# Optimization experiments

Measured on AMD Instinct MI355X. Metric: run time of the kernel, lower is better.

The kernel has to match this reference:

```python
import jax, jax.numpy as jnp
import numpy as np

S, B, T, D, TS, V = 256, 8, 1024, 512, 512, 32000
LN_EPS = 1e-5


def setup_inputs() -> dict:
    key = jax.random.key(0)
    ks = jax.random.split(key, 16)
    std = 0.02
    inp = {
        "outs": jax.random.normal(ks[0], (S, B, D), jnp.float32),
        "graph_state": jax.random.normal(ks[1], (T, B, D), jnp.float32),
        "graph_padding_mask": jnp.zeros((B, T), bool),
        "copy_seq": jax.random.randint(ks[2], (T, B), 0, V),
        # single-head attention projections
        "Wq": std * jax.random.normal(ks[3], (D, D), jnp.float32),
        "bq": jnp.zeros((D,), jnp.float32),
        "Wk": std * jax.random.normal(ks[4], (D, D), jnp.float32),
        "bk": jnp.zeros((D,), jnp.float32),
        "Wv": std * jax.random.normal(ks[5], (D, D), jnp.float32),
        "bv": jnp.zeros((D,), jnp.float32),
        "Wo": std * jax.random.normal(ks[6], (D, D), jnp.float32),
        "bo": jnp.zeros((D,), jnp.float32),
        # layer norm
        "ln_g": jnp.ones((D,), jnp.float32),
        "ln_b": jnp.zeros((D,), jnp.float32),
        # transfer / generator / diverter linears
        "Wt": std * jax.random.normal(ks[7], (TS, D), jnp.float32),
        "bt": jnp.zeros((TS,), jnp.float32),
        "Wgen": std * jax.random.normal(ks[8], (V, TS), jnp.float32),
        "bgen": jnp.zeros((V,), jnp.float32),
        "Wdiv": std * jax.random.normal(ks[9], (2, TS), jnp.float32),
        "bdiv": jnp.zeros((2,), jnp.float32),
    }
    return inp


def _layer_norm(x, g, b):
    mu = jnp.mean(x, -1, keepdims=True)
    var = jnp.mean(jnp.square(x - mu), -1, keepdims=True)
    return (x - mu) * jax.lax.rsqrt(var + LN_EPS) * g + b


def reference(outs, graph_state, graph_padding_mask, copy_seq,
              Wq, bq, Wk, bk, Wv, bv, Wo, bo, ln_g, ln_b,
              Wt, bt, Wgen, bgen, Wdiv, bdiv):
    scale = 1.0 / jnp.sqrt(jnp.asarray(D, outs.dtype))
    q = (outs @ Wq.T + bq) * scale              # [S,B,D]
    k = graph_state @ Wk.T + bk                 # [T,B,D]
    v = graph_state @ Wv.T + bv                 # [T,B,D]
    scores = jnp.einsum("sbd,tbd->sbt", q, k)   # [S,B,T]
    scores = jnp.where(graph_padding_mask[None, :, :], -1e9, scores)
    attn = jax.nn.softmax(scores, axis=-1)      # alignment_weight [S,B,T]
    ctx = jnp.einsum("sbt,tbd->sbd", attn, v)
    x = ctx @ Wo.T + bo
    outs = _layer_norm(outs + x, ln_g, ln_b)
    outs_token = jnp.tanh(outs @ Wt.T + bt)     # [S,B,TS]
    gates = jax.nn.softmax(outs_token @ Wdiv.T + bdiv, axis=-1)
    gen_gate, copy_gate = gates[..., 0:1], gates[..., 1:2]
    probs = gen_gate * jax.nn.softmax(outs_token @ Wgen.T + bgen, axis=-1)  # [S,B,V]
    # copy indices: [T,B] -> [S,B,T] broadcast (indices < V, so no vocab extension)
    index = jnp.broadcast_to(copy_seq.T[None, :, :], (S, B, T))
    copy_probs = copy_gate * attn               # [S,B,T]
    s_idx = jnp.arange(S)[:, None, None]
    b_idx = jnp.arange(B)[None, :, None]
    probs = probs.at[s_idx, b_idx, index].add(copy_probs)
    ll = jnp.log(probs + 1e-12)
    return ll
```

## Files before the change

### kernel.cpp

```cpp
#include <hip/hip_runtime.h>
#include <hip/hip_bf16.h>
#include <math.h>

#define SS 256
#define BB 8
#define TT 1024
#define DD 512
#define TSD 512
#define VV 32000
#define LN_EPS_F 1e-5f
#define VHALF 16000

typedef __attribute__((ext_vector_type(8))) short bf16x8;
typedef __attribute__((ext_vector_type(4))) float f32x4;

__device__ __forceinline__ unsigned short f2bf(float f) {
    union { float f; unsigned int u; } c; c.f = f;
    unsigned int u = c.u;
    return (unsigned short)((u + 0x7fffu + ((u >> 16) & 1u)) >> 16);
}
__device__ __forceinline__ float bf2f(unsigned short s) {
    union { unsigned int u; float f; } c; c.u = ((unsigned int)s) << 16;
    return c.f;
}

__device__ __forceinline__ void glls16(const void* g, void* l) {
    __builtin_amdgcn_global_load_lds(
        (const __attribute__((address_space(1))) unsigned int*)g,
        (__attribute__((address_space(3))) unsigned int*)l,
        16, 0, 0);
}

__device__ __forceinline__ float warp_red_sum(float v) {
    for (int o = 32; o > 0; o >>= 1) v += __shfl_down(v, o, 64);
    return v;
}
__device__ __forceinline__ float warp_red_max(float v) {
    for (int o = 32; o > 0; o >>= 1) v = fmaxf(v, __shfl_down(v, o, 64));
    return v;
}
__device__ __forceinline__ float block_red_sum(float v, float* s) {
    int lane = threadIdx.x & 63, wid = threadIdx.x >> 6;
    v = warp_red_sum(v);
    __syncthreads();
    if (lane == 0) s[wid] = v;
    __syncthreads();
    float r = 0.f;
    int nw = blockDim.x >> 6;
    for (int i = 0; i < nw; i++) r += s[i];
    return r;
}
__device__ __forceinline__ float block_red_max(float v, float* s) {
    int lane = threadIdx.x & 63, wid = threadIdx.x >> 6;
    v = warp_red_max(v);
    __syncthreads();
    if (lane == 0) s[wid] = v;
    __syncthreads();
    float r = s[0];
    int nw = blockDim.x >> 6;
    for (int i = 1; i < nw; i++) r = fmaxf(r, s[i]);
    return r;
}

template<int IN_BF16, int OUT_MODE, int ACT>
__device__ __forceinline__ void gemm_body(
    unsigned short* smem, int bx, int by, int z,
    const void* __restrict__ Ap, long long lda, long long aoff,
    const void* __restrict__ Bp, long long ldb, long long boff,
    const float* __restrict__ bias,
    void* __restrict__ Cp, long long ldc, long long coff,
    int K, float scale, float* __restrict__ rsum)
{
    unsigned short* As = smem;
    unsigned short* Bs = smem + 128 * 64;
    const int tid = threadIdx.x;
    const int lane = tid & 63;
    const int wave = tid >> 6;
    const int wm = (wave >> 1) << 6;
    const int wn = (wave & 1) << 6;
    const int lane15 = lane & 15;
    const int quad = lane >> 4;
    const long long m0 = (long long)bx * 128;
    const long long n0 = (long long)by * 128;

    f32x4 acc[4][4];
#pragma unroll
    for (int i = 0; i < 4; i++)
#pragma unroll
        for (int j = 0; j < 4; j++) acc[i][j] = (f32x4){0.f, 0.f, 0.f, 0.f};

    for (int k0 = 0; k0 < K; k0 += 64) {
        if (IN_BF16) {
            const unsigned short* A = (const unsigned short*)Ap + z * aoff;
            const unsigned short* B = (const unsigned short*)Bp + z * boff;
#pragma unroll
            for (int r = 0; r < 4; r++) {
                int c = r * 256 + tid;
                int row = c >> 3;
                int kc = (c & 7) ^ (row & 7);
                glls16(A + (m0 + row) * lda + k0 + kc * 8, &As[c * 8]);
                glls16(B + (n0 + row) * ldb + k0 + kc * 8, &Bs[c * 8]);
            }
        } else {
            const float* A = (const float*)Ap + z * aoff;
            const float* B = (const float*)Bp + z * boff;
#pragma unroll
            for (int r = 0; r < 4; r++) {
                int c = r * 256 + tid;
                int row = c >> 3;
                int kc = (c & 7) ^ (row & 7);
                const float* ga = A + (m0 + row) * lda + k0 + kc * 8;
                const float* gb = B + (n0 + row) * ldb + k0 + kc * 8;
                float4 a0 = *(const float4*)ga, a1 = *(const float4*)(ga + 4);
                float4 b0 = *(const float4*)gb, b1 = *(const float4*)(gb + 4);
                union { unsigned short us[8]; int4 v; } pa, pb;
                pa.us[0] = f2bf(a0.x); pa.us[1] = f2bf(a0.y); pa.us[2] = f2bf(a0.z); pa.us[3] = f2bf(a0.w);
                pa.us[4] = f2bf(a1.x); pa.us[5] = f2bf(a1.y); pa.us[6] = f2bf(a1.z); pa.us[7] = f2bf(a1.w);
                pb.us[0] = f2bf(b0.x); pb.us[1] = f2bf(b0.y); pb.us[2] = f2bf(b0.z); pb.us[3] = f2bf(b0.w);
                pb.us[4] = f2bf(b1.x); pb.us[5] = f2bf(b1.y); pb.us[6] = f2bf(b1.z); pb.us[7] = f2bf(b1.w);
                *(int4*)&As[c * 8] = pa.v;
                *(int4*)&Bs[c * 8] = pb.v;
            }
        }
        __syncthreads();
#pragma unroll
        for (int s = 0; s < 2; s++) {
            bf16x8 af[4], bfr[4];
#pragma unroll
            for (int i = 0; i < 4; i++) {
                int arow = wm + i * 16 + lane15;
                int kc = (s * 4 + quad) ^ (lane15 & 7);
                af[i] = *(const bf16x8*)&As[(arow * 8 + kc) * 8];
                int brow = wn + i * 16 + lane15;
                bfr[i] = *(const bf16x8*)&Bs[(brow * 8 + kc) * 8];
            }
#pragma unroll
            for (int i = 0; i < 4; i++)
#pragma unroll
                for (int j = 0; j < 4; j++)
                    acc[i][j] = __builtin_amdgcn_mfma_f32_16x16x32_bf16(af[i], bfr[j], acc[i][j], 0, 0, 0);
        }
        __syncthreads();
    }
    const long long zc = z * coff;
    float* sRowF = (float*)&smem[0];
    if (ACT == 2) {
        if (tid < 128) sRowF[tid] = 0.f;
        __syncthreads();
    }
#pragma unroll
    for (int i = 0; i < 4; i++) {
        float rs[4] = {0.f, 0.f, 0.f, 0.f};
#pragma unroll
        for (int j = 0; j < 4; j++) {
            float bv = bias ? bias[n0 + wn + j * 16 + lane15] : 0.f;
#pragma unroll
            for (int r2 = 0; r2 < 4; r2++) {
                float v = (acc[i][j][r2] + bv) * scale;
                if (ACT == 1) v = tanhf(v);
                if (ACT == 2) { v = __expf(v); rs[r2] += v; }
                acc[i][j][r2] = v;
            }
        }
        if (ACT == 2) {
#pragma unroll
            for (int r2 = 0; r2 < 4; r2++) {
                float s = rs[r2];
                s += __shfl_xor(s, 1, 64);
                s += __shfl_xor(s, 2, 64);
                s += __shfl_xor(s, 4, 64);
                s += __shfl_xor(s, 8, 64);
                if (lane15 == 0) atomicAdd(&sRowF[wm + i * 16 + quad * 4 + r2], s);
            }
        }
    }
    if (ACT == 2) {
        __syncthreads();
        if (tid < 128) atomicAdd(rsum + m0 + tid, sRowF[tid]);
        __syncthreads();
    }
    if (OUT_MODE >= 1) {
#pragma unroll
        for (int i = 0; i < 4; i++) {
#pragma unroll
            for (int r2 = 0; r2 < 4; r2++) {
                int lr = wm + i * 16 + quad * 4 + r2;
                int sw = (lr & 7) << 4;
#pragma unroll
                for (int j = 0; j < 4; j++) {
                    int lc = wn + j * 16 + lane15;
                    smem[lr * 128 + (lc ^ sw)] = f2bf(acc[i][j][r2]);
                }
            }
        }
        __syncthreads();
        if (OUT_MODE == 1) {
            unsigned short* Co = (unsigned short*)Cp + zc;
#pragma unroll
            for (int u = 0; u < 8; u++) {
                int e = tid + u * 256;
                int lr = e >> 4, lc8 = e & 15;
                int lcs = (lc8 * 8) ^ ((lr & 7) << 4);
                int4 vv4 = *(const int4*)&smem[lr * 128 + lcs];
                *(int4*)(Co + (m0 + lr) * ldc + n0 + lc8 * 8) = vv4;
            }
        } else {
            unsigned short* vT = (unsigned short*)Cp;
            const int t0g = (int)(m0 >> 3);
#pragma unroll
            for (int u = 0; u < 4; u++) {
                int e = tid + u * 256;
                int b = e >> 7, dl = e & 127;
                int sw = (b & 7) << 4;
                union { unsigned short us[16]; int4 v[2]; } pk;
#pragma unroll
                for (int tl = 0; tl < 16; tl++)
                    pk.us[tl] = smem[(tl * 8 + b) * 128 + (dl ^ sw)];
                unsigned short* dst = vT + (long long)b * (DD * TT) + (long long)(n0 + dl) * TT + t0g;
                *(int4*)dst = pk.v[0];
                *(int4*)(dst + 8) = pk.v[1];
            }
        }
        __syncthreads();
    } else {
#pragma unroll
        for (int i = 0; i < 4; i++) {
            long long rbase = m0 + wm + i * 16 + quad * 4;
#pragma unroll
            for (int j = 0; j < 4; j++) {
                long long col = n0 + wn + j * 16 + lane15;
#pragma unroll
                for (int r2 = 0; r2 < 4; r2++)
                    ((float*)Cp)[zc + (rbase + r2) * ldc + col] = acc[i][j][r2];
            }
        }
    }
}

template<int IN_BF16, int OUT_MODE, int ACT, int SWZ>
__global__ __launch_bounds__(256) void mfma_gemm(
    const void* __restrict__ Ap, long long lda, long long aoff,
    const void* __restrict__ Bp, long long ldb, long long boff,
    const float* __restrict__ bias,
    void* __restrict__ Cp, long long ldc, long long coff,
    int K, float scale, float* __restrict__ rsum)
{
    __shared__ __align__(16) unsigned short smem[2 * 128 * 64];
    int bx = blockIdx.x, by = blockIdx.y;
    if (SWZ) {
        unsigned int nx = gridDim.x;
        unsigned int nwg = nx * gridDim.y;
        unsigned int lin = blockIdx.y * nx + blockIdx.x;
        unsigned int q = nwg >> 3, r = nwg & 7u;
        unsigned int xcd = lin & 7u, loc = lin >> 3;
        unsigned int wg = (xcd < r ? xcd * (q + 1u) : r * (q + 1u) + (xcd - r) * q) + loc;
        bx = (int)(wg % nx);
        by = (int)(wg / nx);
    }
    gemm_body<IN_BF16, OUT_MODE, ACT>(smem, bx, by, blockIdx.z,
        Ap, lda, aoff, Bp, ldb, boff, bias, Cp, ldc, coff, K, scale, rsum);
}

__global__ __launch_bounds__(256) void front_fused(
    const float* __restrict__ outs, const float* __restrict__ Wq, const float* __restrict__ bq,
    const float* __restrict__ gstate, const float* __restrict__ Wk, const float* __restrict__ bk,
    const float* __restrict__ Wv, const float* __restrict__ bv,
    unsigned short* __restrict__ qb, unsigned short* __restrict__ kb,
    unsigned short* __restrict__ vTb,
    const float* __restrict__ Wgen, unsigned short* __restrict__ wgenb,
    float* __restrict__ gs, float qscale)
{
    extern __shared__ __align__(16) unsigned short dsm[];
    const int bid = blockIdx.x;
    if (bid < 64) {
        gemm_body<0, 1, 0>(dsm, bid & 15, bid >> 4, 0,
            outs, 512, 0, Wq, 512, 0, bq, qb, 512, 0, 512, qscale, nullptr);
    } else if (bid < 320) {
        int lb = bid - 64;
        gemm_body<0, 1, 0>(dsm, lb & 63, lb >> 6, 0,
            gstate, 512, 0, Wk, 512, 0, bk, kb, 512, 0, 512, 1.f, nullptr);
    } else if (bid < 576) {
        int lb = bid - 320;
        gemm_body<0, 2, 0>(dsm, lb & 63, lb >> 6, 0,
            gstate, 512, 0, Wv, 512, 0, bv, vTb, 0, 0, 512, 1.f, nullptr);
    } else {
        int lb = bid - 576;
        if (lb < 8) gs[lb * 256 + threadIdx.x] = 0.f;
        long long i = (long long)lb * 256 + threadIdx.x;
        const float4* p = (const float4*)Wgen + i * 2;
        float4 a = p[0], b = p[1];
        union { unsigned short us[8]; int4 v; } pk;
        pk.us[0] = f2bf(a.x); pk.us[1] = f2bf(a.y); pk.us[2] = f2bf(a.z); pk.us[3] = f2bf(a.w);
        pk.us[4] = f2bf(b.x); pk.us[5] = f2bf(b.y); pk.us[6] = f2bf(b.z); pk.us[7] = f2bf(b.w);
        ((int4*)wgenb)[i] = pk.v;
    }
}

__global__ __launch_bounds__(256) void attn_softmax(
    float* __restrict__ scores, unsigned short* __restrict__ scores_bf,
    const unsigned char* __restrict__ mask)
{
    __shared__ float red[4];
    int row = blockIdx.x;
    int b = row & (BB - 1);
    float* p = scores + (long long)row * TT;
    unsigned short* pb = scores_bf + (long long)row * TT;
    const unsigned char* mr = mask + (long long)b * TT;
    float vals[TT / 256];
    float lmax = -3.0e38f;
#pragma unroll
    for (int i = 0; i < TT / 256; i++) {
        int t = threadIdx.x + i * 256;
        float s = p[t];
        if (mr[t]) s = -1.0e9f;
        vals[i] = s;
        lmax = fmaxf(lmax, s);
    }
    float gmax = block_red_max(lmax, red);
    float lsum = 0.f;
#pragma unroll
    for (int i = 0; i < TT / 256; i++) {
        vals[i] = __expf(vals[i] - gmax);
        lsum += vals[i];
    }
    float gsum = block_red_sum(lsum, red);
    float inv = 1.f / gsum;
#pragma unroll
    for (int i = 0; i < TT / 256; i++) {
        float v = vals[i] * inv;
        int t = threadIdx.x + i * 256;
        p[t] = v;
        pb[t] = f2bf(v);
    }
}

__global__ __launch_bounds__(256) void add_ln(
    const float* __restrict__ outs, const float* __restrict__ xo,
    const float* __restrict__ g, const float* __restrict__ bln,
    float* __restrict__ y)
{
    __shared__ float red[4];
    int row = blockIdx.x;
    const float* o = outs + (long long)row * DD;
    const float* xp = xo + (long long)row * DD;
    float x[DD / 256];
    float s = 0.f;
#pragma unroll
    for (int i = 0; i < DD / 256; i++) {
        int d = threadIdx.x + i * 256;
        x[i] = o[d] + xp[d];
        s += x[i];
    }
    float mu = block_red_sum(s, red) * (1.f / DD);
    float s2 = 0.f;
#pragma unroll
    for (int i = 0; i < DD / 256; i++) {
        float dv = x[i] - mu;
        s2 += dv * dv;
    }
    float var = block_red_sum(s2, red) * (1.f / DD);
    float rinv = rsqrtf(var + LN_EPS_F);
#pragma unroll
    for (int i = 0; i < DD / 256; i++) {
        int d = threadIdx.x + i * 256;
        y[(long long)row * DD + d] = (x[i] - mu) * rinv * g[d] + bln[d];
    }
}

__global__ __launch_bounds__(512) void copy_log_final(
    const unsigned short* __restrict__ eb, const float* __restrict__ attn,
    const unsigned short* __restrict__ tok, const float* __restrict__ Wdiv,
    const float* __restrict__ bdiv, const float* __restrict__ gs,
    const int* __restrict__ seq, float* __restrict__ out)
{
    __shared__ __align__(16) float pc[VHALF];
    __shared__ float red[8];
    const int tid = threadIdx.x;
    const int row = blockIdx.x;
    const int half = blockIdx.y;
    const int base = half * VHALF;
    const int b = row & (BB - 1);

    for (int i = tid; i < VHALF; i += 512) pc[i] = 0.f;

    float tv = bf2f(tok[(long long)row * TSD + tid]);
    float a0 = tv * Wdiv[tid];
    float a1 = tv * Wdiv[TSD + tid];
    a0 = block_red_sum(a0, red);
    a1 = block_red_sum(a1, red);
    a0 += bdiv[0];
    a1 += bdiv[1];
    float mx = fmaxf(a0, a1);
    float e0 = __expf(a0 - mx), e1 = __expf(a1 - mx);
    float inv2 = 1.f / (e0 + e1);
    const float cv = e1 * inv2;
    const float ginv = (e0 * inv2) / gs[row];
    __syncthreads();

    const float* arow = attn + (long long)row * TT;
#pragma unroll
    for (int it = 0; it < 2; it++) {
        int t = tid + it * 512;
        int idx = seq[t * BB + b];
        int loc = idx - base;
        if (loc >= 0 && loc < VHALF)
            atomicAdd(&pc[loc], cv * arow[t]);
    }
    __syncthreads();

    const unsigned short* erow = eb + (long long)row * VV + base;
    float* orow = out + (long long)row * VV + base;
    const float4* pc4 = (const float4*)pc;
    for (int c = tid; c < VHALF / 8; c += 512) {
        bf16x8 ev = *(const bf16x8*)(erow + c * 8);
        float4 p0 = pc4[c * 2], p1 = pc4[c * 2 + 1];
        float4 o0, o1;
        o0.x = __logf(fmaf(bf2f((unsigned short)ev[0]), ginv, p0.x) + 1e-12f);
        o0.y = __logf(fmaf(bf2f((unsigned short)ev[1]), ginv, p0.y) + 1e-12f);
        o0.z = __logf(fmaf(bf2f((unsigned short)ev[2]), ginv, p0.z) + 1e-12f);
        o0.w = __logf(fmaf(bf2f((unsigned short)ev[3]), ginv, p0.w) + 1e-12f);
        o1.x = __logf(fmaf(bf2f((unsigned short)ev[4]), ginv, p1.x) + 1e-12f);
        o1.y = __logf(fmaf(bf2f((unsigned short)ev[5]), ginv, p1.y) + 1e-12f);
        o1.z = __logf(fmaf(bf2f((unsigned short)ev[6]), ginv, p1.z) + 1e-12f);
        o1.w = __logf(fmaf(bf2f((unsigned short)ev[7]), ginv, p1.w) + 1e-12f);
        ((float4*)orow)[c * 2] = o0;
        ((float4*)orow)[c * 2 + 1] = o1;
    }
}

extern "C" void kernel_launch(void* const* d_in, const int* in_sizes, int n_in,
                              void* d_out, int out_size, void* d_ws, size_t ws_size,
                              hipStream_t stream)
{
    const float* outs = (const float*)d_in[0];
    const float* gstate = (const float*)d_in[1];
    const unsigned char* mask = (const unsigned char*)d_in[2];
    const int* seq = (const int*)d_in[3];
    const float* Wq = (const float*)d_in[4];  const float* bq = (const float*)d_in[5];
    const float* Wk = (const float*)d_in[6];  const float* bk = (const float*)d_in[7];
    const float* Wv = (const float*)d_in[8];  const float* bv = (const float*)d_in[9];
    const float* Wo = (const float*)d_in[10]; const float* bo = (const float*)d_in[11];
    const float* lng = (const float*)d_in[12]; const float* lnb = (const float*)d_in[13];
    const float* Wt = (const float*)d_in[14]; const float* bt = (const float*)d_in[15];
    const float* Wgen = (const float*)d_in[16]; const float* bgen = (const float*)d_in[17];
    const float* Wdiv = (const float*)d_in[18]; const float* bdiv = (const float*)d_in[19];
    float* out = (float*)d_out;

    char* w = (char*)d_ws;
    unsigned short* qb    = (unsigned short*)w; w += 2048LL * 512 * 2;
    unsigned short* kb    = (unsigned short*)w; w += 8192LL * 512 * 2;
    unsigned short* tokb  = (unsigned short*)w; w += 2048LL * 512 * 2;
    unsigned short* wgenb = (unsigned short*)w; w += 32000LL * 512 * 2;
    unsigned short* vTb   = (unsigned short*)w; w += 8LL * 512 * 1024 * 2;
    unsigned short* attnb = (unsigned short*)w; w += 2048LL * 1024 * 2;
    unsigned short* eb    = (unsigned short*)w; w += 2048LL * 32000 * 2;
    float* attn = (float*)w; w += 2048LL * 1024 * 4;
    float* ctx  = (float*)w; w += 2048LL * 512 * 4;
    float* xo   = (float*)w; w += 2048LL * 512 * 4;
    float* y    = (float*)w; w += 2048LL * 512 * 4;
    float* gs   = (float*)w; w += 2048 * 4;

    float qscale = 1.0f / sqrtf((float)DD);
    dim3 blk(256);

    front_fused<<<8576, blk, 32768, stream>>>(outs, Wq, bq, gstate, Wk, bk, Wv, bv,
                                              qb, kb, vTb, Wgen, wgenb, gs, qscale);
    mfma_gemm<1, 0, 0, 0><<<dim3(2, 8, 8), blk, 0, stream>>>(qb, 4096, 512, kb, 4096, 512, nullptr, attn, 8192, 1024, 512, 1.f, nullptr);
    attn_softmax<<<2048, blk, 0, stream>>>(attn, attnb, mask);
    mfma_gemm<1, 0, 0, 0><<<dim3(2, 4, 8), blk, 0, stream>>>(attnb, 8192, 1024, vTb, 1024, 524288, nullptr, ctx, 4096, 512, 1024, 1.f, nullptr);
    mfma_gemm<0, 0, 0, 0><<<dim3(16, 4, 1), blk, 0, stream>>>(ctx, 512, 0, Wo, 512, 0, bo, xo, 512, 0, 512, 1.f, nullptr);
    add_ln<<<2048, blk, 0, stream>>>(outs, xo, lng, lnb, y);
    mfma_gemm<0, 1, 1, 0><<<dim3(16, 4, 1), blk, 0, stream>>>(y, 512, 0, Wt, 512, 0, bt, tokb, 512, 0, 512, 1.f, nullptr);
    mfma_gemm<1, 1, 2, 1><<<dim3(16, 250, 1), blk, 0, stream>>>(tokb, 512, 0, wgenb, 512, 0, bgen, eb, 32000, 0, 512, 1.f, gs);
    copy_log_final<<<dim3(2048, 2), dim3(512), 0, stream>>>(eb, attn, tokb, Wdiv, bdiv, gs, seq, out);
}
```

Before: 702.3 us.

## Split-K the attention GEMMs and fuse residual-add LayerNorm into neighbouring GEMMs

The QK^T and attn·V batched GEMMs now use split-K over two halves, writing two partial fp32 buffers to double the block count on small grids. The partials are summed in the softmax load and in the A-load of the Wo GEMM. The Wo GEMM epilogue adds the residual, writes the sum, and atomically accumulates per-row sum and sum-of-squares. The next GEMM then applies LayerNorm on its A tile during load, which removes the separate add_ln kernel. The fp32 attention writeback is dropped and the copy scatter reads bf16 attention, saving traffic at the cost of single-pass variance precision and bf16 copy probabilities.

```diff
diff --git a/kernel.cpp b/kernel.cpp
--- a/kernel.cpp
+++ b/kernel.cpp
@@ -62,14 +62,18 @@
     return r;
 }
 
-template<int IN_BF16, int OUT_MODE, int ACT>
+template<int IN_BF16, int OUT_MODE, int ACT, int LN_A, int DUALA>
 __device__ __forceinline__ void gemm_body(
     unsigned short* smem, int bx, int by, int z,
-    const void* __restrict__ Ap, long long lda, long long aoff,
+    const void* __restrict__ Ap, const void* __restrict__ Ap2,
+    long long lda, long long aoff,
     const void* __restrict__ Bp, long long ldb, long long boff,
     const float* __restrict__ bias,
     void* __restrict__ Cp, long long ldc, long long coff,
-    int K, float scale, float* __restrict__ rsum)
+    int K, float scale, float* __restrict__ rsum, float* __restrict__ rsum2,
+    const float* __restrict__ outsP,
+    const float* __restrict__ lnrs, const float* __restrict__ lnrss,
+    const float* __restrict__ lng, const float* __restrict__ lnbp)
 {
     unsigned short* As = smem;
     unsigned short* Bs = smem + 128 * 64;
@@ -113,6 +117,30 @@
                 const float* gb = B + (n0 + row) * ldb + k0 + kc * 8;
                 float4 a0 = *(const float4*)ga, a1 = *(const float4*)(ga + 4);
                 float4 b0 = *(const float4*)gb, b1 = *(const float4*)(gb + 4);
+                if (DUALA) {
+                    const float* ga2 = (const float*)Ap2 + z * aoff + (m0 + row) * lda + k0 + kc * 8;
+                    float4 c0 = *(const float4*)ga2, c1 = *(const float4*)(ga2 + 4);
+                    a0.x += c0.x; a0.y += c0.y; a0.z += c0.z; a0.w += c0.w;
+                    a1.x += c1.x; a1.y += c1.y; a1.z += c1.z; a1.w += c1.w;
+                }
+                if (LN_A) {
+                    long long grow = m0 + row;
+                    float mu = lnrs[grow] * (1.f / DD);
+                    float var = lnrss[grow] * (1.f / DD) - mu * mu;
+                    float rinv = rsqrtf(var + LN_EPS_F);
+                    const float* gp = lng + k0 + kc * 8;
+                    const float* bp = lnbp + k0 + kc * 8;
+                    float4 g0 = *(const float4*)gp, g1 = *(const float4*)(gp + 4);
+                    float4 e0 = *(const float4*)bp, e1 = *(const float4*)(bp + 4);
+                    a0.x = (a0.x - mu) * rinv * g0.x + e0.x;
+                    a0.y = (a0.y - mu) * rinv * g0.y + e0.y;
+                    a0.z = (a0.z - mu) * rinv * g0.z + e0.z;
+                    a0.w = (a0.w - mu) * rinv * g0.w + e0.w;
+                    a1.x = (a1.x - mu) * rinv * g1.x + e1.x;
+                    a1.y = (a1.y - mu) * rinv * g1.y + e1.y;
+                    a1.z = (a1.z - mu) * rinv * g1.z + e1.z;
+                    a1.w = (a1.w - mu) * rinv * g1.w + e1.w;
+                }
                 union { unsigned short us[8]; int4 v; } pa, pb;
                 pa.us[0] = f2bf(a0.x); pa.us[1] = f2bf(a0.y); pa.us[2] = f2bf(a0.z); pa.us[3] = f2bf(a0.w);
                 pa.us[4] = f2bf(a1.x); pa.us[5] = f2bf(a1.y); pa.us[6] = f2bf(a1.z); pa.us[7] = f2bf(a1.w);
@@ -148,29 +176,51 @@
         if (tid < 128) sRowF[tid] = 0.f;
         __syncthreads();
     }
+    if (ACT == 3) {
+        if (tid < 256) sRowF[tid] = 0.f;
+        __syncthreads();
+    }
 #pragma unroll
     for (int i = 0; i < 4; i++) {
-        float rs[4] = {0.f, 0.f, 0.f, 0.f};
+        const long long rbase = m0 + wm + i * 16 + quad * 4;
+        float rs_[4] = {0.f, 0.f, 0.f, 0.f};
+        float rq_[4] = {0.f, 0.f, 0.f, 0.f};
 #pragma unroll
         for (int j = 0; j < 4; j++) {
-            float bv = bias ? bias[n0 + wn + j * 16 + lane15] : 0.f;
+            long long col = n0 + wn + j * 16 + lane15;
+            float bv = bias ? bias[col] : 0.f;
 #pragma unroll
             for (int r2 = 0; r2 < 4; r2++) {
                 float v = (acc[i][j][r2] + bv) * scale;
                 if (ACT == 1) v = tanhf(v);
-                if (ACT == 2) { v = __expf(v); rs[r2] += v; }
+                if (ACT == 2) { v = __expf(v); rs_[r2] += v; }
+                if (ACT == 3) {
+                    long long idx = zc + (rbase + r2) * ldc + col;
+                    v += outsP[idx];
+                    ((float*)Cp)[idx] = v;
+                    rs_[r2] += v;
+                    rq_[r2] += v * v;
+                }
                 acc[i][j][r2] = v;
             }
         }
-        if (ACT == 2) {
+        if (ACT == 2 || ACT == 3) {
 #pragma unroll
             for (int r2 = 0; r2 < 4; r2++) {
-                float s = rs[r2];
+                float s = rs_[r2];
                 s += __shfl_xor(s, 1, 64);
                 s += __shfl_xor(s, 2, 64);
                 s += __shfl_xor(s, 4, 64);
                 s += __shfl_xor(s, 8, 64);
                 if (lane15 == 0) atomicAdd(&sRowF[wm + i * 16 + quad * 4 + r2], s);
+                if (ACT == 3) {
+                    float q = rq_[r2];
+                    q += __shfl_xor(q, 1, 64);
+                    q += __shfl_xor(q, 2, 64);
+                    q += __shfl_xor(q, 4, 64);
+                    q += __shfl_xor(q, 8, 64);
+                    if (lane15 == 0) atomicAdd(&sRowF[128 + wm + i * 16 + quad * 4 + r2], q);
+                }
             }
         }
     }
@@ -178,6 +228,14 @@
         __syncthreads();
         if (tid < 128) atomicAdd(rsum + m0 + tid, sRowF[tid]);
         __syncthreads();
+    }
+    if (ACT == 3) {
+        __syncthreads();
+        if (tid < 128) {
+            atomicAdd(rsum + m0 + tid, sRowF[tid]);
+            atomicAdd(rsum2 + m0 + tid, sRowF[128 + tid]);
+        }
+        return;
     }
     if (OUT_MODE >= 1) {
 #pragma unroll
@@ -237,13 +295,17 @@
     }
 }
 
-template<int IN_BF16, int OUT_MODE, int ACT, int SWZ>
+template<int IN_BF16, int OUT_MODE, int ACT, int LN_A, int DUALA, int SWZ>
 __global__ __launch_bounds__(256) void mfma_gemm(
-    const void* __restrict__ Ap, long long lda, long long aoff,
+    const void* __restrict__ Ap, const void* __restrict__ Ap2,
+    long long lda, long long aoff,
     const void* __restrict__ Bp, long long ldb, long long boff,
     const float* __restrict__ bias,
     void* __restrict__ Cp, long long ldc, long long coff,
-    int K, float scale, float* __restrict__ rsum)
+    int K, float scale, float* __restrict__ rsum, float* __restrict__ rsum2,
+    const float* __restrict__ outsP,
+    const float* __restrict__ lnrs, const float* __restrict__ lnrss,
+    const float* __restrict__ lng, const float* __restrict__ lnbp)
 {
     __shared__ __align__(16) unsigned short smem[2 * 128 * 64];
     int bx = blockIdx.x, by = blockIdx.y;
@@ -257,8 +319,25 @@
         bx = (int)(wg % nx);
         by = (int)(wg / nx);
     }
-    gemm_body<IN_BF16, OUT_MODE, ACT>(smem, bx, by, blockIdx.z,
-        Ap, lda, aoff, Bp, ldb, boff, bias, Cp, ldc, coff, K, scale, rsum);
+    gemm_body<IN_BF16, OUT_MODE, ACT, LN_A, DUALA>(smem, bx, by, blockIdx.z,
+        Ap, Ap2, lda, aoff, Bp, ldb, boff, bias, Cp, ldc, coff, K, scale,
+        rsum, rsum2, outsP, lnrs, lnrss, lng, lnbp);
+}
+
+__global__ __launch_bounds__(256) void mfma_gemm_splitk(
+    const unsigned short* __restrict__ Ap, long long lda, long long aoff,
+    const unsigned short* __restrict__ Bp, long long ldb, long long boff,
+    float* __restrict__ C0, float* __restrict__ C1,
+    long long ldc, long long coff, int Khalf)
+{
+    __shared__ __align__(16) unsigned short smem[2 * 128 * 64];
+    int b = blockIdx.z & 7, kz = blockIdx.z >> 3;
+    const unsigned short* A = Ap + (long long)kz * Khalf;
+    const unsigned short* B = Bp + (long long)kz * Khalf;
+    float* C = kz ? C1 : C0;
+    gemm_body<1, 0, 0, 0, 0>(smem, blockIdx.x, blockIdx.y, b,
+        A, nullptr, lda, aoff, B, ldb, boff, nullptr, C, ldc, coff, Khalf, 1.f,
+        nullptr, nullptr, nullptr, nullptr, nullptr, nullptr, nullptr);
 }
 
 __global__ __launch_bounds__(256) void front_fused(
@@ -268,24 +347,31 @@
     unsigned short* __restrict__ qb, unsigned short* __restrict__ kb,
     unsigned short* __restrict__ vTb,
     const float* __restrict__ Wgen, unsigned short* __restrict__ wgenb,
-    float* __restrict__ gs, float qscale)
+    float* __restrict__ gs, float* __restrict__ rs, float* __restrict__ rss,
+    float qscale)
 {
     extern __shared__ __align__(16) unsigned short dsm[];
     const int bid = blockIdx.x;
     if (bid < 64) {
-        gemm_body<0, 1, 0>(dsm, bid & 15, bid >> 4, 0,
-            outs, 512, 0, Wq, 512, 0, bq, qb, 512, 0, 512, qscale, nullptr);
+        gemm_body<0, 1, 0, 0, 0>(dsm, bid & 15, bid >> 4, 0,
+            outs, nullptr, 512, 0, Wq, 512, 0, bq, qb, 512, 0, 512, qscale,
+            nullptr, nullptr, nullptr, nullptr, nullptr, nullptr, nullptr);
     } else if (bid < 320) {
         int lb = bid - 64;
-        gemm_body<0, 1, 0>(dsm, lb & 63, lb >> 6, 0,
-            gstate, 512, 0, Wk, 512, 0, bk, kb, 512, 0, 512, 1.f, nullptr);
+        gemm_body<0, 1, 0, 0, 0>(dsm, lb & 63, lb >> 6, 0,
+            gstate, nullptr, 512, 0, Wk, 512, 0, bk, kb, 512, 0, 512, 1.f,
+            nullptr, nullptr, nullptr, nullptr, nullptr, nullptr, nullptr);
     } else if (bid < 576) {
         int lb = bid - 320;
-        gemm_body<0, 2, 0>(dsm, lb & 63, lb >> 6, 0,
-            gstate, 512, 0, Wv, 512, 0, bv, vTb, 0, 0, 512, 1.f, nullptr);
+        gemm_body<0, 2, 0, 0, 0>(dsm, lb & 63, lb >> 6, 0,
+            gstate, nullptr, 512, 0, Wv, 512, 0, bv, vTb, 0, 0, 512, 1.f,
+            nullptr, nullptr, nullptr, nullptr, nullptr, nullptr, nullptr);
     } else {
         int lb = bid - 576;
-        if (lb < 8) gs[lb * 256 + threadIdx.x] = 0.f;
+        if (lb < 8) {
+            int i = lb * 256 + threadIdx.x;
+            gs[i] = 0.f; rs[i] = 0.f; rss[i] = 0.f;
+        }
         long long i = (long long)lb * 256 + threadIdx.x;
         const float4* p = (const float4*)Wgen + i * 2;
         float4 a = p[0], b = p[1];
@@ -297,13 +383,14 @@
 }
 
 __global__ __launch_bounds__(256) void attn_softmax(
-    float* __restrict__ scores, unsigned short* __restrict__ scores_bf,
-    const unsigned char* __restrict__ mask)
+    const float* __restrict__ s0, const float* __restrict__ s1,
+    unsigned short* __restrict__ scores_bf, const unsigned char* __restrict__ mask)
 {
     __shared__ float red[4];
     int row = blockIdx.x;
     int b = row & (BB - 1);
-    float* p = scores + (long long)row * TT;
+    const float* p0 = s0 + (long long)row * TT;
+    const float* p1 = s1 + (long long)row * TT;
     unsigned short* pb = scores_bf + (long long)row * TT;
     const unsigned char* mr = mask + (long long)b * TT;
     float vals[TT / 256];
@@ -311,7 +398,7 @@
 #pragma unroll
     for (int i = 0; i < TT / 256; i++) {
         int t = threadIdx.x + i * 256;
-        float s = p[t];
+        float s = p0[t] + p1[t];
         if (mr[t]) s = -1.0e9f;
         vals[i] = s;
         lmax = fmaxf(lmax, s);
@@ -326,49 +413,12 @@
     float gsum = block_red_sum(lsum, red);
     float inv = 1.f / gsum;
 #pragma unroll
-    for (int i = 0; i < TT / 256; i++) {
-        float v = vals[i] * inv;
-        int t = threadIdx.x + i * 256;
-        p[t] = v;
-        pb[t] = f2bf(v);
-    }
-}
-
-__global__ __launch_bounds__(256) void add_ln(
-    const float* __restrict__ outs, const float* __restrict__ xo,
-    const float* __restrict__ g, const float* __restrict__ bln,
-    float* __restrict__ y)
-{
-    __shared__ float red[4];
-    int row = blockIdx.x;
-    const float* o = outs + (long long)row * DD;
-    const float* xp = xo + (long long)row * DD;
-    float x[DD / 256];
-    float s = 0.f;
-#pragma unroll
-    for (int i = 0; i < DD / 256; i++) {
-        int d = threadIdx.x + i * 256;
-        x[i] = o[d] + xp[d];
-        s += x[i];
-    }
-    float mu = block_red_sum(s, red) * (1.f / DD);
-    float s2 = 0.f;
-#pragma unroll
-    for (int i = 0; i < DD / 256; i++) {
-        float dv = x[i] - mu;
-        s2 += dv * dv;
-    }
-    float var = block_red_sum(s2, red) * (1.f / DD);
-    float rinv = rsqrtf(var + LN_EPS_F);
-#pragma unroll
-    for (int i = 0; i < DD / 256; i++) {
-        int d = threadIdx.x + i * 256;
-        y[(long long)row * DD + d] = (x[i] - mu) * rinv * g[d] + bln[d];
-    }
+    for (int i = 0; i < TT / 256; i++)
+        pb[threadIdx.x + i * 256] = f2bf(vals[i] * inv);
 }
 
 __global__ __launch_bounds__(512) void copy_log_final(
-    const unsigned short* __restrict__ eb, const float* __restrict__ attn,
+    const unsigned short* __restrict__ eb, const unsigned short* __restrict__ attnb,
     const unsigned short* __restrict__ tok, const float* __restrict__ Wdiv,
     const float* __restrict__ bdiv, const float* __restrict__ gs,
     const int* __restrict__ seq, float* __restrict__ out)
@@ -397,14 +447,14 @@
     const float ginv = (e0 * inv2) / gs[row];
     __syncthreads();
 
-    const float* arow = attn + (long long)row * TT;
+    const unsigned short* arow = attnb + (long long)row * TT;
 #pragma unroll
     for (int it = 0; it < 2; it++) {
         int t = tid + it * 512;
         int idx = seq[t * BB + b];
         int loc = idx - base;
         if (loc >= 0 && loc < VHALF)
-            atomicAdd(&pc[loc], cv * arow[t]);
+            atomicAdd(&pc[loc], cv * bf2f(arow[t]));
     }
     __syncthreads();
 
@@ -454,23 +504,33 @@
     unsigned short* vTb   = (unsigned short*)w; w += 8LL * 512 * 1024 * 2;
     unsigned short* attnb = (unsigned short*)w; w += 2048LL * 1024 * 2;
     unsigned short* eb    = (unsigned short*)w; w += 2048LL * 32000 * 2;
-    float* attn = (float*)w; w += 2048LL * 1024 * 4;
-    float* ctx  = (float*)w; w += 2048LL * 512 * 4;
-    float* xo   = (float*)w; w += 2048LL * 512 * 4;
-    float* y    = (float*)w; w += 2048LL * 512 * 4;
-    float* gs   = (float*)w; w += 2048 * 4;
+    float* attn0 = (float*)w; w += 2048LL * 1024 * 4;
+    float* attn1 = (float*)w; w += 2048LL * 1024 * 4;
+    float* ctx0  = (float*)w; w += 2048LL * 512 * 4;
+    float* ctx1  = (float*)w; w += 2048LL * 512 * 4;
+    float* sres  = (float*)w; w += 2048LL * 512 * 4;
+    float* gs    = (float*)w; w += 2048 * 4;
+    float* rs    = (float*)w; w += 2048 * 4;
+    float* rss   = (float*)w; w += 2048 * 4;
 
     float qscale = 1.0f / sqrtf((float)DD);
     dim3 blk(256);
 
     front_fused<<<8576, blk, 32768, stream>>>(outs, Wq, bq, gstate, Wk, bk, Wv, bv,
-                                              qb, kb, vTb, Wgen, wgenb, gs, qscale);
-    mfma_gemm<1, 0, 0, 0><<<dim3(2, 8, 8), blk, 0, stream>>>(qb, 4096, 512, kb, 4096, 512, nullptr, attn, 8192, 1024, 512, 1.f, nullptr);
-    attn_softmax<<<2048, blk, 0, stream>>>(attn, attnb, mask);
-    mfma_gemm<1, 0, 0, 0><<<dim3(2, 4, 8), blk, 0, stream>>>(attnb, 8192, 1024, vTb, 1024, 524288, nullptr, ctx, 4096, 512, 1024, 1.f, nullptr);
-    mfma_gemm<0, 0, 0, 0><<<dim3(16, 4, 1), blk, 0, stream>>>(ctx, 512, 0, Wo, 512, 0, bo, xo, 512, 0, 512, 1.f, nullptr);
-    add_ln<<<2048, blk, 0, stream>>>(outs, xo, lng, lnb, y);
-    mfma_gemm<0, 1, 1, 0><<<dim3(16, 4, 1), blk, 0, stream>>>(y, 512, 0, Wt, 512, 0, bt, tokb, 512, 0, 512, 1.f, nullptr);
-    mfma_gemm<1, 1, 2, 1><<<dim3(16, 250, 1), blk, 0, stream>>>(tokb, 512, 0, wgenb, 512, 0, bgen, eb, 32000, 0, 512, 1.f, gs);
-    copy_log_final<<<dim3(2048, 2), dim3(512), 0, stream>>>(eb, attn, tokb, Wdiv, bdiv, gs, seq, out);
-}
+                                              qb, kb, vTb, Wgen, wgenb, gs, rs, rss, qscale);
+    mfma_gemm_splitk<<<dim3(2, 8, 16), blk, 0, stream>>>(qb, 4096, 512, kb, 4096, 512,
+                                                         attn0, attn1, 8192, 1024, 256);
+    attn_softmax<<<2048, blk, 0, stream>>>(attn0, attn1, attnb, mask);
+    mfma_gemm_splitk<<<dim3(2, 4, 16), blk, 0, stream>>>(attnb, 8192, 1024, vTb, 1024, 524288,
+                                                         ctx0, ctx1, 4096, 512, 512);
+    mfma_gemm<0, 0, 3, 0, 1, 0><<<dim3(16, 4, 1), blk, 0, stream>>>(
+        ctx0, ctx1, 512, 0, Wo, 512, 0, bo, sres, 512, 0, 512, 1.f,
+        rs, rss, outs, nullptr, nullptr, nullptr, nullptr);
+    mfma_gemm<0, 1, 1, 1, 0, 0><<<dim3(16, 4, 1), blk, 0, stream>>>(
+        sres, nullptr, 512, 0, Wt, 512, 0, bt, tokb, 512, 0, 512, 1.f,
+        nullptr, nullptr, nullptr, rs, rss, lng, lnb);
+    mfma_gemm<1, 1, 2, 0, 0, 1><<<dim3(16, 250, 1), blk, 0, stream>>>(
+        tokb, nullptr, 512, 0, wgenb, 512, 0, bgen, eb, 32000, 0, 512, 1.f,
+        gs, nullptr, nullptr, nullptr, nullptr, nullptr, nullptr);
+    copy_log_final<<<dim3(2048, 2), dim3(512), 0, stream>>>(eb, attnb, tokb, Wdiv, bdiv, gs, seq, out);
+}
```

Measured after the change: 684.1 us. 1.03x faster.
